# Performance work log

Hardware: AMD Instinct MI355X
Metric: run time of the kernel (lower is better)

## Reference

```python
import jax, jax.numpy as jnp
import numpy as np

B, N = 8, 2048          # clouds x points per cloud
M1, M2 = 1024, 256      # centroids after ratio 0.5, then 0.25
K = 64                  # max_num_neighbors
R1, R2 = 0.2, 0.4       # radii
CURV_K = 10             # knn for curvature
CURV_SCALAR = 10.0      # Net(curvature_scalar)
NEG = -1e30


def _sqdist(a, b):
    # squared pairwise distances [len(a), len(b)] without an [.,.,3] intermediate
    return jnp.sum(a * a, -1)[:, None] + jnp.sum(b * b, -1)[None, :] - 2.0 * (a @ b.T)


def _mlp3(x, Wa, ba, Wb, bb, Wc, bc):
    # torch_geometric MLP: Linear+ReLU hidden layers, plain last layer
    h = jax.nn.relu(x @ Wa + ba)
    h = jax.nn.relu(h @ Wb + bb)
    return h @ Wc + bc


def _curvature(pos):
    # per-point surface variation lambda_min / sum(lambda) over k-NN covariance
    d2 = _sqdist(pos, pos)                        # [N,N]
    _, idx = jax.lax.top_k(-d2, CURV_K)           # k nearest (incl. self)
    nbr = pos[idx]                                # [N,k,3]
    c = nbr - jnp.mean(nbr, 1, keepdims=True)
    cov = jnp.einsum('nki,nkj->nij', c, c) / CURV_K
    ev = jnp.linalg.eigvalsh(cov)                 # ascending
    return ev[:, 0] / (jnp.sum(ev, -1) + 1e-8)


def _fps_weighted(pos, curv, m):
    # farthest point sampling, min-distance score weighted by curvature
    w = 1.0 + CURV_SCALAR * curv
    d0 = jnp.sum((pos - pos[0]) ** 2, -1)
    def step(min_d2, _):
        i = jnp.argmax(min_d2 * w)
        nd = jnp.sum((pos - pos[i]) ** 2, -1)
        return jnp.minimum(min_d2, nd), i
    _, rest = jax.lax.scan(step, d0, None, length=m - 1)
    return jnp.concatenate([jnp.zeros((1,), rest.dtype), rest])


def _sa(x, pos, curv, m, r, params):
    # SAModule: weighted FPS -> radius grouping (cap K) -> PointNetConv (gather, MLP, max)
    idx = _fps_weighted(pos, curv, m)
    cpos = pos[idx]                               # [m,3]
    d2 = _sqdist(cpos, pos)                       # [m,N]
    score = jnp.where(d2 <= r * r, -d2, NEG)
    vals, nidx = jax.lax.top_k(score, K)          # up to K nearest within radius
    mask = vals > NEG * 0.5                       # [m,K]
    rel = pos[nidx] - cpos[:, None, :]            # [m,K,3]
    feats = rel if x is None else jnp.concatenate([x[nidx], rel], -1)
    msg = _mlp3(feats, *params)                   # [m,K,F]
    msg = jnp.where(mask[:, :, None], msg, NEG)
    out = jnp.max(msg, 1)                         # scatter-max aggregation
    out = jnp.where(jnp.any(mask, 1)[:, None], out, 0.0)  # empty groups -> 0
    return out, cpos, curv[idx]


def _forward(pos, W1a, b1a, W1b, b1b, W1c, b1c, W2a, b2a, W2b, b2b, W2c, b2c,
             W3a, b3a, W3b, b3b, W3c, b3c, Wh1, bh1, Wh2, bh2, Wh3, bh3):
    p1 = (W1a, b1a, W1b, b1b, W1c, b1c)
    p2 = (W2a, b2a, W2b, b2b, W2c, b2c)
    p3 = (W3a, b3a, W3b, b3b, W3c, b3c)
    def cloud(p):
        curv = _curvature(p)
        x1, pos1, c1 = _sa(None, p, curv, M1, R1, p1)
        x2, pos2, _ = _sa(x1, pos1, c1, M2, R2, p2)
        g = _mlp3(jnp.concatenate([x2, pos2], -1), *p3)   # [M2,1024]
        return jnp.max(g, 0)                              # global max pool
    gfeat = jax.vmap(cloud)(pos.reshape(B, N, 3))          # [B,1024]
    logits = _mlp3(gfeat, Wh1, bh1, Wh2, bh2, Wh3, bh3)    # dropout (eval) = id
    return jax.nn.log_softmax(logits, -1)


_LAYERS = [("W1a", "b1a", 3, 64), ("W1b", "b1b", 64, 64), ("W1c", "b1c", 64, 128),
           ("W2a", "b2a", 131, 128), ("W2b", "b2b", 128, 128), ("W2c", "b2c", 128, 256),
           ("W3a", "b3a", 259, 256), ("W3b", "b3b", 256, 512), ("W3c", "b3c", 512, 1024),
           ("Wh1", "bh1", 1024, 512), ("Wh2", "bh2", 512, 256), ("Wh3", "bh3", 256, 10)]


def setup_inputs() -> dict:
    key = jax.random.key(0)
    ks = iter(jax.random.split(key, 2 * len(_LAYERS) + 1))
    inp = {"pos": jax.random.uniform(next(ks), (B * N, 3), jnp.float32)}
    for wn, bn, fi, fo in _LAYERS:
        inp[wn] = jax.random.normal(next(ks), (fi, fo), jnp.float32) / np.sqrt(fi)
        inp[bn] = jnp.zeros((fo,), jnp.float32)
    return inp


def reference(pos, W1a, b1a, W1b, b1b, W1c, b1c, W2a, b2a, W2b, b2b, W2c, b2c,
              W3a, b3a, W3b, b3b, W3c, b3c, Wh1, bh1, Wh2, bh2, Wh3, bh3):
    return _forward(pos, W1a, b1a, W1b, b1b, W1c, b1c, W2a, b2a, W2b, b2b, W2c, b2c,
                    W3a, b3a, W3b, b3b, W3c, b3c, Wh1, bh1, Wh2, bh2, Wh3, bh3)
```

## Files before the change

### kernel.cpp

```cpp
#include <hip/hip_runtime.h>
#include <hip/hip_fp16.h>
#include <math.h>

#define TID threadIdx.x

typedef _Float16 h2vec __attribute__((ext_vector_type(2)));
typedef _Float16 f16x8 __attribute__((ext_vector_type(8)));
typedef float f32x4 __attribute__((ext_vector_type(4)));
typedef float f32x2v __attribute__((ext_vector_type(2)));

#if __has_builtin(__builtin_elementwise_fma)
#define EFMA(a, b, c) __builtin_elementwise_fma((a), (b), (c))
#else
static __device__ __forceinline__ f32x2v EFMA(f32x2v a, f32x2v b, f32x2v c) {
    f32x2v r;
    r.x = fmaf(a.x, b.x, c.x);
    r.y = fmaf(a.y, b.y, c.y);
    return r;
}
#endif

static __device__ __forceinline__ float fdot2(unsigned a, unsigned b, float c) {
    h2vec av, bv;
    __builtin_memcpy(&av, &a, 4);
    __builtin_memcpy(&bv, &b, 4);
    return __builtin_amdgcn_fdot2(av, bv, c, false);
}

static __device__ __forceinline__ unsigned packh2(float a, float b) {
    __half2 hh = __floats2half2_rn(a, b);
    unsigned u;
    __builtin_memcpy(&u, &hh, 4);
    return u;
}

static __device__ __forceinline__ unsigned encf(float f) {
    unsigned u = __float_as_uint(f);
    return (u >> 31) ? ~u : (u | 0x80000000u);
}
static __device__ __forceinline__ float decf(unsigned e) {
    unsigned u = (e >> 31) ? (e & 0x7fffffffu) : ~e;
    return __uint_as_float(u);
}

static __device__ __forceinline__ int wave_sum(int v) {
    v += __builtin_amdgcn_update_dpp(0, v, 0x111, 0xf, 0xf, true);
    v += __builtin_amdgcn_update_dpp(0, v, 0x112, 0xf, 0xf, true);
    v += __builtin_amdgcn_update_dpp(0, v, 0x114, 0xf, 0xf, true);
    v += __builtin_amdgcn_update_dpp(0, v, 0x118, 0xf, 0xf, true);
    v += __builtin_amdgcn_update_dpp(0, v, 0x142, 0xf, 0xf, true);
    v += __builtin_amdgcn_update_dpp(0, v, 0x143, 0xf, 0xf, true);
    return __builtin_amdgcn_readlane(v, 63);
}

template <int CTRL>
static __device__ __forceinline__ unsigned long long dpp_max_u64(unsigned long long k) {
    int lo = (int)(unsigned)(k & 0xffffffffULL);
    int hi = (int)(unsigned)(k >> 32);
    int lo2 = __builtin_amdgcn_update_dpp(0, lo, CTRL, 0xf, 0xf, true);
    int hi2 = __builtin_amdgcn_update_dpp(0, hi, CTRL, 0xf, 0xf, true);
    unsigned long long k2 = ((unsigned long long)(unsigned)hi2 << 32) | (unsigned)lo2;
    return k2 > k ? k2 : k;
}

static __device__ __forceinline__ void pack_slot(const float* __restrict__ W,
                                                 unsigned* __restrict__ out,
                                                 int K, int ncols, int t) {
    int lane = t & 63;
    int frag = t >> 6;
    int nct = ncols >> 4;
    int ks = frag / nct, ct = frag - ks * nct;
    int kbase = (ks << 5) + ((lane >> 4) << 3);
    int cc = (ct << 4) + (lane & 15);
    unsigned o[4];
#pragma unroll
    for (int i = 0; i < 4; ++i) {
        int k0 = kbase + 2 * i, k1 = kbase + 2 * i + 1;
        float f0 = (k0 < K) ? W[(size_t)k0 * ncols + cc] : 0.f;
        float f1 = (k1 < K) ? W[(size_t)k1 * ncols + cc] : 0.f;
        o[i] = packh2(f0, f1);
    }
    *(uint4*)&out[(size_t)t * 4] = make_uint4(o[0], o[1], o[2], o[3]);
}

__global__ __launch_bounds__(256) void curv_kernel(const float* __restrict__ pos,
                                                   float* __restrict__ curv) {
    __shared__ float4 sp[2048];
    __shared__ float smd[64][40];
    __shared__ int smi[64][40];
    int cloud = blockIdx.x >> 5;
    int base = cloud << 11;
    for (int j = TID; j < 2048; j += 256) {
        const float* p = pos + (size_t)(base + j) * 3;
        float x = p[0], y = p[1], z = p[2];
        sp[j] = make_float4(x, y, z, fmaf(x, x, fmaf(y, y, z * z)));
    }
    __syncthreads();
    int pt = TID >> 2;
    int sub = TID & 3;
    int li = ((blockIdx.x & 31) << 6) + pt;
    float4 pi = sp[li];
    float bd[10];
    int bi[10];
#pragma unroll
    for (int t = 0; t < 10; ++t) { bd[t] = 3.0e38f; bi[t] = 0; }
    int j0 = sub << 9;
    for (int jj = 0; jj < 512; ++jj) {
        int j = j0 + jj;
        float4 pj = sp[j];
        float dot = fmaf(pi.x, pj.x, fmaf(pi.y, pj.y, pi.z * pj.z));
        float d2 = pi.w + pj.w - 2.0f * dot;
        if (d2 < bd[9]) {
            bd[9] = d2; bi[9] = j;
#pragma unroll
            for (int t = 9; t > 0; --t) {
                if (bd[t] < bd[t - 1]) {
                    float td = bd[t]; bd[t] = bd[t - 1]; bd[t - 1] = td;
                    int ti = bi[t]; bi[t] = bi[t - 1]; bi[t - 1] = ti;
                }
            }
        }
    }
#pragma unroll
    for (int t = 0; t < 10; ++t) {
        smd[pt][sub * 10 + t] = bd[t];
        smi[pt][sub * 10 + t] = bi[t];
    }
    __syncthreads();
    float d0 = smd[pt][0], d1 = smd[pt][10], d2h = smd[pt][20], d3 = smd[pt][30];
    int i0 = smi[pt][0], i1 = smi[pt][10], i2 = smi[pt][20], i3 = smi[pt][30];
    int h0 = 0, h1 = 0, h2c = 0, h3 = 0;
    int mbi[10];
#pragma unroll
    for (int t = 0; t < 10; ++t) {
        bool a01 = (d1 < d0) || (d1 == d0 && i1 < i0);
        float dA = a01 ? d1 : d0; int iA = a01 ? i1 : i0;
        bool a23 = (d3 < d2h) || (d3 == d2h && i3 < i2);
        float dB = a23 ? d3 : d2h; int iB = a23 ? i3 : i2;
        bool ab = (dB < dA) || (dB == dA && iB < iA);
        mbi[t] = ab ? iB : iA;
        if (ab) {
            if (a23) { ++h3; d3 = (h3 < 10) ? smd[pt][30 + h3] : 3.0e38f;
                       i3 = (h3 < 10) ? smi[pt][30 + h3] : 0x7fffffff; }
            else     { ++h2c; d2h = (h2c < 10) ? smd[pt][20 + h2c] : 3.0e38f;
                       i2 = (h2c < 10) ? smi[pt][20 + h2c] : 0x7fffffff; }
        } else {
            if (a01) { ++h1; d1 = (h1 < 10) ? smd[pt][10 + h1] : 3.0e38f;
                       i1 = (h1 < 10) ? smi[pt][10 + h1] : 0x7fffffff; }
            else     { ++h0; d0 = (h0 < 10) ? smd[pt][h0] : 3.0e38f;
                       i0 = (h0 < 10) ? smi[pt][h0] : 0x7fffffff; }
        }
    }
    if (sub != 0) return;
    double sx = 0, sy = 0, sz = 0;
#pragma unroll
    for (int t = 0; t < 10; ++t) { float4 p = sp[mbi[t]]; sx += p.x; sy += p.y; sz += p.z; }
    double mx = sx / 10.0, my = sy / 10.0, mz = sz / 10.0;
    double cxx = 0, cxy = 0, cxz = 0, cyy = 0, cyz = 0, czz = 0;
#pragma unroll
    for (int t = 0; t < 10; ++t) {
        float4 p = sp[mbi[t]];
        double dx = p.x - mx, dy = p.y - my, dz = p.z - mz;
        cxx += dx * dx; cxy += dx * dy; cxz += dx * dz;
        cyy += dy * dy; cyz += dy * dz; czz += dz * dz;
    }
    cxx /= 10.0; cxy /= 10.0; cxz /= 10.0; cyy /= 10.0; cyz /= 10.0; czz /= 10.0;
    double q = (cxx + cyy + czz) / 3.0;
    double b00 = cxx - q, b11 = cyy - q, b22 = czz - q;
    double p2 = b00 * b00 + b11 * b11 + b22 * b22 +
                2.0 * (cxy * cxy + cxz * cxz + cyz * cyz);
    double lmin;
    if (p2 <= 0.0) {
        lmin = q;
    } else {
        double p = sqrt(p2 / 6.0);
        double inv = 1.0 / p;
        double c00 = b00 * inv, c01 = cxy * inv, c02 = cxz * inv;
        double c11 = b11 * inv, c12 = cyz * inv, c22 = b22 * inv;
        double detB = c00 * (c11 * c22 - c12 * c12)
                    - c01 * (c01 * c22 - c12 * c02)
                    + c02 * (c01 * c12 - c11 * c02);
        double r = 0.5 * detB;
        r = fmin(1.0, fmax(-1.0, r));
        double phi = acos(r) / 3.0;
        lmin = q + 2.0 * p * cos(phi + 2.0943951023931953);
    }
    double s3 = cxx + cyy + czz;
    curv[base + li] = (float)(lmin / (s3 + 1e-8));
}

template <int N, int M, int SLOTS>
static __device__ void fps_body(
    const float* __restrict__ srcpos, int stride, const float* __restrict__ srccurv,
    int cloud, float4* __restrict__ outPos, float* __restrict__ outCurv,
    float* __restrict__ outA, int ldA,
    float4* sp, int* sidx, unsigned long long* rec ) {
    constexpr int PAIRS = SLOTS / 2;
    const float* cp = srcpos + (size_t)cloud * N * stride;
    for (int j = TID; j < N; j += 256)
        sp[j] = make_float4(cp[j * stride], cp[j * stride + 1], cp[j * stride + 2], 0.f);
    if (TID == 0) sidx[0] = 0;
    __syncthreads();
    f32x2v px[PAIRS], py[PAIRS], pz[PAIRS], md[PAIRS], wvv[PAIRS];
#pragma unroll
    for (int s = 0; s < PAIRS; ++s) {
        int p0 = ((2 * s) << 8) + TID, p1 = ((2 * s + 1) << 8) + TID;
        float4 q0 = sp[p0], q1 = sp[p1];
        px[s].x = q0.x; px[s].y = q1.x;
        py[s].x = q0.y; py[s].y = q1.y;
        pz[s].x = q0.z; pz[s].y = q1.z;
        md[s].x = 3.0e38f; md[s].y = 3.0e38f;
        wvv[s].x = fmaf(10.0f, srccurv[cloud * N + p0], 1.0f);
        wvv[s].y = fmaf(10.0f, srccurv[cloud * N + p1], 1.0f);
    }
    int lane = TID & 63, w4 = TID >> 6;
    float4 c0 = sp[0];
    float cx = c0.x, cy = c0.y, cz = c0.z;
    for (int t = 1; t < M; ++t) {
        f32x2v cxv, cyv, czv;
        cxv.x = cx; cxv.y = cx; cyv.x = cy; cyv.y = cy; czv.x = cz; czv.y = cz;
        unsigned long long kk[PAIRS];
#pragma unroll
        for (int s = 0; s < PAIRS; ++s) {
            f32x2v dx = px[s] - cxv, dy = py[s] - cyv, dz = pz[s] - czv;
            f32x2v nd = EFMA(dx, dx, EFMA(dy, dy, dz * dz));
            f32x2v m2 = __builtin_elementwise_min(md[s], nd);
            md[s] = m2;
            f32x2v sc = m2 * wvv[s];
            unsigned long long k0 =
                ((unsigned long long)__float_as_uint(sc.x) << 32) |
                (unsigned)(2047 - (((2 * s) << 8) + TID));
            unsigned long long k1 =
                ((unsigned long long)__float_as_uint(sc.y) << 32) |
                (unsigned)(2047 - (((2 * s + 1) << 8) + TID));
            kk[s] = k0 > k1 ? k0 : k1;
        }
        unsigned long long k = kk[0];
#pragma unroll
        for (int s = 1; s < PAIRS; ++s) k = kk[s] > k ? kk[s] : k;
        k = dpp_max_u64<0x111>(k);
        k = dpp_max_u64<0x112>(k);
        k = dpp_max_u64<0x114>(k);
        k = dpp_max_u64<0x118>(k);
        k = dpp_max_u64<0x142>(k);
        k = dpp_max_u64<0x143>(k);
        int pbase = (t & 1) << 2;
        if (lane == 63) rec[pbase | w4] = k;
        __syncthreads();
        unsigned long long k0 = rec[pbase + 0];
        unsigned long long k1 = rec[pbase + 1];
        unsigned long long k2 = rec[pbase + 2];
        unsigned long long k3 = rec[pbase + 3];
        unsigned long long ka = k0 > k1 ? k0 : k1;
        unsigned long long kb = k2 > k3 ? k2 : k3;
        unsigned long long km = ka > kb ? ka : kb;
        int nbix = 2047 - (int)(unsigned)(km & 0xffffffffULL);
        if (TID == 0) sidx[t] = nbix;
        float4 cc = sp[nbix];
        cx = cc.x; cy = cc.y; cz = cc.z;
    }
    __syncthreads();
    for (int j = TID; j < M; j += 256) {
        int id = sidx[j];
        float4 qv = sp[id];
        outPos[cloud * M + j] = qv;
        if (outCurv) outCurv[cloud * M + j] = srccurv[cloud * N + id];
        if (outA) {
            float* a = outA + (size_t)(cloud * M + j) * ldA;
            a[256] = qv.x; a[257] = qv.y; a[258] = qv.z;
        }
    }
}

__global__ __launch_bounds__(256, 1) void fps1_pack_kernel(
    const float* __restrict__ pos, const float* __restrict__ curv,
    float4* __restrict__ pos1, float* __restrict__ curv1,
    const float* __restrict__ Wc, const float* __restrict__ Wa,
    const float* __restrict__ Wb, const float* __restrict__ W3a,
    const float* __restrict__ W3b, const float* __restrict__ W3c,
    unsigned* __restrict__ WcH, unsigned* __restrict__ WaH,
    unsigned* __restrict__ WbH, unsigned* __restrict__ W3aH,
    unsigned* __restrict__ W3bH, unsigned* __restrict__ W3cH,
    unsigned* __restrict__ gfeatE) {
    __shared__ float4 sp[2048];
    __shared__ int sidx[1024];
    __shared__ unsigned long long rec[8];
    if (blockIdx.x < 8) {
        fps_body<2048, 1024, 8>(pos, 3, curv, blockIdx.x, pos1, curv1, nullptr, 0,
                                sp, sidx, rec);
        return;
    }
    int b = blockIdx.x - 8;
    if (b == 0)
        for (int i = TID; i < 8192; i += 256) gfeatE[i] = 0u;
    if (b < 16)        pack_slot(Wc,  WcH,  128, 256,  b * 256 + TID);
    else if (b < 26)   pack_slot(Wa,  WaH,  131, 128,  (b - 16) * 256 + TID);
    else if (b < 34)   pack_slot(Wb,  WbH,  128, 128,  (b - 26) * 256 + TID);
    else if (b < 70)   pack_slot(W3a, W3aH, 259, 256,  (b - 34) * 256 + TID);
    else if (b < 134)  pack_slot(W3b, W3bH, 256, 512,  (b - 70) * 256 + TID);
    else               pack_slot(W3c, W3cH, 512, 1024, (b - 134) * 256 + TID);
}

static __device__ __forceinline__ int select_k64(const unsigned int* ck, const int* ci,
                                                 int c, int lane, int* cnt2, int* sel,
                                                 int* nbOut) {
    if (c <= 64) {
        *nbOut = c;
        return (lane < c) ? ci[lane] : 0;
    }
    unsigned int T = 0;
    for (int bit = 31; bit >= 0; --bit) {
        unsigned int mid = T | (1u << bit);
        int cl = 0;
        for (int q = lane; q < c; q += 64) cl += (ck[q] < mid) ? 1 : 0;
        if (wave_sum(cl) < 64) T = mid;
    }
    int cl = 0;
    for (int q = lane; q < c; q += 64) cl += (ck[q] < T) ? 1 : 0;
    int need = 64 - wave_sum(cl);
    int TI = 0;
    for (int bit = 11; bit >= 0; --bit) {
        int mid = TI | (1 << bit);
        int ce = 0;
        for (int q = lane; q < c; q += 64) ce += (ck[q] == T && ci[q] < mid) ? 1 : 0;
        if (wave_sum(ce) < need) TI = mid;
    }
    for (int q = lane; q < c; q += 64) {
        unsigned int kq = ck[q];
        int iq = ci[q];
        if (kq < T || (kq == T && iq <= TI)) sel[atomicAdd(cnt2, 1)] = iq;
    }
    *nbOut = 64;
    return sel[lane];
}

static __device__ __forceinline__ int select_k64_fast(
    const unsigned* __restrict__ ck, const int* __restrict__ ci,
    int c, int lane, int* sel, int* nbOut) {
    if (c <= 64) {
        *nbOut = c;
        return (lane < c) ? ci[lane] : 0;
    }
    unsigned long long kq[4];
    bool act[4];
#pragma unroll
    for (int q = 0; q < 4; ++q) {
        int idx = (q << 6) + lane;
        bool v = idx < c;
        act[q] = v;
        kq[q] = v ? (((unsigned long long)ck[idx] << 32) | (unsigned)ci[idx]) : 0ULL;
    }
    int excess = c - 64;
    if (excess <= 24) {
        for (int r = 0; r < excess; ++r) {
            unsigned long long k = 0;
#pragma unroll
            for (int q = 0; q < 4; ++q) {
                unsigned long long kc = act[q] ? kq[q] : 0ULL;
                k = kc > k ? kc : k;
            }
            k = dpp_max_u64<0x111>(k);
            k = dpp_max_u64<0x112>(k);
            k = dpp_max_u64<0x114>(k);
            k = dpp_max_u64<0x118>(k);
            k = dpp_max_u64<0x142>(k);
            k = dpp_max_u64<0x143>(k);
            unsigned klo = (unsigned)__builtin_amdgcn_readlane(
                (int)(unsigned)(k & 0xffffffffULL), 63);
            unsigned khi = (unsigned)__builtin_amdgcn_readlane(
                (int)(unsigned)(k >> 32), 63);
            unsigned long long km = ((unsigned long long)khi << 32) | klo;
#pragma unroll
            for (int q = 0; q < 4; ++q)
                if (act[q] && kq[q] == km) act[q] = false;
        }
    } else {
        unsigned T = 0;
        for (int bit = 31; bit >= 0; --bit) {
            unsigned mid = T | (1u << bit);
            int cl = 0;
#pragma unroll
            for (int q = 0; q < 4; ++q)
                cl += (act[q] && (unsigned)(kq[q] >> 32) < mid) ? 1 : 0;
            if (wave_sum(cl) < 64) T = mid;
        }
        int cl = 0;
#pragma unroll
        for (int q = 0; q < 4; ++q)
            cl += (act[q] && (unsigned)(kq[q] >> 32) < T) ? 1 : 0;
        int need = 64 - wave_sum(cl);
        int TI = 0;
        for (int bit = 11; bit >= 0; --bit) {
            int mid = TI | (1 << bit);
            int ce = 0;
#pragma unroll
            for (int q = 0; q < 4; ++q)
                ce += (act[q] && (unsigned)(kq[q] >> 32) == T &&
                       (int)(unsigned)(kq[q] & 0xffffffffULL) < mid) ? 1 : 0;
            if (wave_sum(ce) < need) TI = mid;
        }
#pragma unroll
        for (int q = 0; q < 4; ++q) {
            unsigned hi = (unsigned)(kq[q] >> 32);
            int lo = (int)(unsigned)(kq[q] & 0xffffffffULL);
            act[q] = act[q] && (hi < T || (hi == T && lo <= TI));
        }
    }
    int base = 0;
#pragma unroll
    for (int q = 0; q < 4; ++q) {
        unsigned long long m = __ballot(act[q]);
        if (act[q]) {
            int off = __popcll(m & ((1ULL << lane) - 1));
            sel[base + off] = (int)(unsigned)(kq[q] & 0xffffffffULL);
        }
        base += __popcll(m);
    }
    *nbOut = 64;
    return sel[lane];
}

union U1 {
    struct {
        float4 sp[2048];
        unsigned ck[4][256];
        int ci[4][256];
        int sel[4][64];
    } p;
    unsigned h2s[4][2048];
};

static __device__ void conv1_body(
    int bid, U1& u,
    const float* __restrict__ pos, const float4* __restrict__ pos1,
    const float* __restrict__ W1, const float* __restrict__ B1,
    const float* __restrict__ W2, const float* __restrict__ B2,
    const float* __restrict__ W3, const float* __restrict__ B3,
    float* __restrict__ x1) {
    __shared__ int nbs[4];
    int cloud = bid >> 8;
    int w4 = TID >> 6, lane = TID & 63;
    int centb = (bid & 255) << 2;
    int g = (cloud << 10) + centb + w4;
    int base = cloud << 11;
    for (int j = TID; j < 2048; j += 256) {
        const float* p = pos + (size_t)(base + j) * 3;
        u.p.sp[j] = make_float4(p[0], p[1], p[2], 0.f);
    }
    __syncthreads();
    float4 cq = pos1[g];
    double cx = cq.x, cy = cq.y, cz = cq.z;
    int cnt = 0;
    for (int s = 0; s < 32; ++s) {
        int j = (s << 6) + lane;
        float4 pj = u.p.sp[j];
        double dx = (double)pj.x - cx, dy = (double)pj.y - cy, dz = (double)pj.z - cz;
        double d2 = dx * dx + dy * dy + dz * dz;
        bool in = (d2 <= 0.2 * 0.2);
        unsigned long long m = __ballot(in);
        if (in) {
            int p = cnt + __popcll(m & ((1ULL << lane) - 1));
            if (p < 256) {
                u.p.ck[w4][p] = __float_as_uint((float)d2);
                u.p.ci[w4][p] = j;
            }
        }
        cnt += __popcll(m);
    }
    int c = min(cnt, 256);
    int nb;
    int idxn = select_k64_fast(u.p.ck[w4], u.p.ci[w4], c, lane, u.p.sel[w4], &nb);
    if (lane == 0) nbs[w4] = nb;
    float4 pn = u.p.sp[idxn];
    float rx = pn.x - cq.x, ry = pn.y - cq.y, rz = pn.z - cq.z;
    __syncthreads();
    float h1[64];
#pragma unroll
    for (int cc2 = 0; cc2 < 64; ++cc2) {
        float v = fmaf(rx, W1[cc2], fmaf(ry, W1[64 + cc2], fmaf(rz, W1[128 + cc2], B1[cc2])));
        h1[cc2] = fmaxf(v, 0.f);
    }
#pragma unroll 1
    for (int half = 0; half < 2; ++half) {
        int c0 = half << 5;
        float h2[32];
#pragma unroll
        for (int t = 0; t < 32; ++t) h2[t] = B2[c0 + t];
#pragma unroll
        for (int i = 0; i < 64; ++i) {
            float hv = h1[i];
            const float* wr = W2 + i * 64 + c0;
#pragma unroll
            for (int t = 0; t < 32; ++t) h2[t] = fmaf(hv, wr[t], h2[t]);
        }
#pragma unroll
        for (int t = 0; t < 32; ++t) h2[t] = fmaxf(h2[t], 0.f);
        unsigned* hrow = &u.h2s[w4][lane << 5];
        int sw = (lane & 7) << 2;
#pragma unroll
        for (int q = 0; q < 4; ++q) {
            unsigned tmp[4];
#pragma unroll
            for (int k2 = 0; k2 < 4; ++k2) {
                int jp = (q << 2) + k2;
                tmp[k2] = packh2(h2[2 * jp], h2[2 * jp + 1]);
            }
            int qg = (half << 2) + q;
            *(uint4*)&hrow[(qg << 2) ^ sw] = make_uint4(tmp[0], tmp[1], tmp[2], tmp[3]);
        }
    }
    __syncthreads();
    int ch = ((w4 & 1) << 6) + lane;
    int cbase = (w4 >> 1) << 1;
    unsigned w2[32];
#pragma unroll
    for (int p = 0; p < 32; ++p)
        w2[p] = packh2(W3[(2 * p) * 128 + ch], W3[(2 * p + 1) * 128 + ch]);
    float bv = B3[ch];
#pragma unroll 1
    for (int ci2 = 0; ci2 < 2; ++ci2) {
        int cc = cbase + ci2;
        int nbc = nbs[cc];
        float m = -1e30f;
        for (int n = 0; n < nbc; ++n) {
            const unsigned* hr = &u.h2s[cc][n << 5];
            int sw2 = (n & 7) << 2;
            float a0 = 0.f, a1 = 0.f, a2 = 0.f, a3 = 0.f;
#pragma unroll
            for (int q = 0; q < 8; ++q) {
                uint4 hv = *(const uint4*)&hr[(q << 2) ^ sw2];
                a0 = fdot2(hv.x, w2[(q << 2) + 0], a0);
                a1 = fdot2(hv.y, w2[(q << 2) + 1], a1);
                a2 = fdot2(hv.z, w2[(q << 2) + 2], a2);
                a3 = fdot2(hv.w, w2[(q << 2) + 3], a3);
            }
            m = fmaxf(m, bv + (a0 + a1) + (a2 + a3));
        }
        x1[(size_t)((cloud << 10) + centb + cc) * 128 + ch] = m;
    }
}

union UM {
    U1 c;
    struct {
        float4 sp[1024];
        unsigned long long rec[8];
        int sidx[256];
    } f;
};

__global__ __launch_bounds__(256, 3) void fps2_conv1_kernel(
    const float* __restrict__ pos, const float4* __restrict__ pos1,
    const float* __restrict__ curv1, float4* __restrict__ pos2,
    float* __restrict__ Abuf,
    const float* __restrict__ W1, const float* __restrict__ B1,
    const float* __restrict__ W2, const float* __restrict__ B2,
    const float* __restrict__ W3, const float* __restrict__ B3,
    float* __restrict__ x1) {
    __shared__ UM u;
    if (blockIdx.x < 8) {
        fps_body<1024, 256, 4>((const float*)pos1, 4, curv1, blockIdx.x, pos2,
                               nullptr, Abuf, 260, u.f.sp, u.f.sidx, u.f.rec);
    } else {
        conv1_body(blockIdx.x - 8, u.c, pos, pos1, W1, B1, W2, B2, W3, B3, x1);
    }
}

union U2 {
    struct {
        float4 sp[1024];
        unsigned ck[4][512];
        int ci[4][512];
        int sel[4][64];
        int cnt[4], cnt2[4];
    } p;
    unsigned xs[4][5376];
};

__global__ __launch_bounds__(256, 1) void conv2_kernel(
    const float4* __restrict__ pos1, const float4* __restrict__ pos2,
    const float* __restrict__ x1,
    const unsigned* __restrict__ WaH, const float* __restrict__ Ba,
    const unsigned* __restrict__ WbH, const float* __restrict__ Bb,
    const unsigned* __restrict__ WcH, const float* __restrict__ Bc,
    float* __restrict__ Aout) {
    __shared__ U2 u;
    __shared__ unsigned h1s[4][4352];
    __shared__ int nbs[4];
    int cloud = blockIdx.x >> 6;
    int w4 = TID >> 6, lane = TID & 63;
    int centb = (blockIdx.x & 63) << 2;
    int g = (cloud << 8) + centb + w4;
    int quad = lane >> 4, l15 = lane & 15;
    for (int j = TID; j < 1024; j += 256) u.p.sp[j] = pos1[(cloud << 10) + j];
    if (lane == 0) { u.p.cnt[w4] = 0; u.p.cnt2[w4] = 0; }
    __syncthreads();
    float4 cq = pos2[g];
    double cx = cq.x, cy = cq.y, cz = cq.z;
    for (int s = 0; s < 16; ++s) {
        int j = (s << 6) + lane;
        float4 pj = u.p.sp[j];
        double dx = (double)pj.x - cx, dy = (double)pj.y - cy, dz = (double)pj.z - cz;
        double d2 = dx * dx + dy * dy + dz * dz;
        if (d2 <= 0.4 * 0.4) {
            int p = atomicAdd(&u.p.cnt[w4], 1);
            if (p < 512) { u.p.ck[w4][p] = __float_as_uint((float)d2); u.p.ci[w4][p] = j; }
        }
    }
    __syncthreads();
    int c = min(u.p.cnt[w4], 512);
    int nb;
    int idxn = select_k64(u.p.ck[w4], u.p.ci[w4], c, lane, &u.p.cnt2[w4],
                          u.p.sel[w4], &nb);
    if (lane == 0) nbs[w4] = nb;
    float4 pn = u.p.sp[idxn];
    float rx = pn.x - cq.x, ry = pn.y - cq.y, rz = pn.z - cq.z;
    __syncthreads();
    {
        const float4* xr = (const float4*)(x1 + (size_t)((cloud << 10) + idxn) * 128);
        unsigned* row = &u.xs[w4][lane * 84];
#pragma unroll
        for (int q = 0; q < 16; ++q) {
            float4 a = xr[q * 2], b = xr[q * 2 + 1];
            *(uint4*)&row[q << 2] = make_uint4(packh2(a.x, a.y), packh2(a.z, a.w),
                                               packh2(b.x, b.y), packh2(b.z, b.w));
        }
        *(uint4*)&row[64] = make_uint4(packh2(rx, ry), packh2(rz, 0.f), 0u, 0u);
        *(uint4*)&row[68] = make_uint4(0u, 0u, 0u, 0u);
        *(uint4*)&row[72] = make_uint4(0u, 0u, 0u, 0u);
        *(uint4*)&row[76] = make_uint4(0u, 0u, 0u, 0u);
    }
    float ba8[8];
#pragma unroll
    for (int ct = 0; ct < 8; ++ct) ba8[ct] = Ba[(ct << 4) + l15];
#pragma unroll 1
    for (int ct = 0; ct < 8; ++ct) {
        f16x8 bfrag[5];
#pragma unroll
        for (int ks = 0; ks < 5; ++ks) {
            uint4 bv = *(const uint4*)&WaH[(size_t)((((ks << 3) | ct) << 6) | lane) << 2];
            __builtin_memcpy(&bfrag[ks], &bv, 16);
        }
#pragma unroll
        for (int rt = 0; rt < 4; ++rt) {
            f32x4 acc = {0.f, 0.f, 0.f, 0.f};
#pragma unroll
            for (int ks = 0; ks < 5; ++ks) {
                f16x8 af;
                uint4 av = *(const uint4*)&u.xs[w4][((rt << 4) + l15) * 84 +
                                                    (((ks << 2) + quad) << 2)];
                __builtin_memcpy(&af, &av, 16);
                acc = __builtin_amdgcn_mfma_f32_16x16x32_f16(af, bfrag[ks], acc, 0, 0, 0);
            }
#pragma unroll
            for (int r = 0; r < 4; ++r) {
                float v = fmaxf(acc[r] + ba8[ct], 0.f);
                float vp = __shfl_xor(v, 1, 64);
                if (!(l15 & 1)) {
                    int rowi = (rt << 4) + (quad << 2) + r;
                    h1s[w4][rowi * 68 + (ct << 3) + (l15 >> 1)] = packh2(v, vp);
                }
            }
        }
    }
    unsigned* h2w = &u.xs[w4][0];
#pragma unroll
    for (int ct = 0; ct < 8; ++ct) ba8[ct] = Bb[(ct << 4) + l15];
#pragma unroll 1
    for (int ct = 0; ct < 8; ++ct) {
        f16x8 bfrag[4];
#pragma unroll
        for (int ks = 0; ks < 4; ++ks) {
            uint4 bv = *(const uint4*)&WbH[(size_t)((((ks << 3) | ct) << 6) | lane) << 2];
            __builtin_memcpy(&bfrag[ks], &bv, 16);
        }
#pragma unroll
        for (int rt = 0; rt < 4; ++rt) {
            f32x4 acc = {0.f, 0.f, 0.f, 0.f};
#pragma unroll
            for (int ks = 0; ks < 4; ++ks) {
                f16x8 af;
                uint4 av = *(const uint4*)&h1s[w4][((rt << 4) + l15) * 68 +
                                                   (((ks << 2) + quad) << 2)];
                __builtin_memcpy(&af, &av, 16);
                acc = __builtin_amdgcn_mfma_f32_16x16x32_f16(af, bfrag[ks], acc, 0, 0, 0);
            }
#pragma unroll
            for (int r = 0; r < 4; ++r) {
                float v = fmaxf(acc[r] + ba8[ct], 0.f);
                float vp = __shfl_xor(v, 1, 64);
                if (!(l15 & 1)) {
                    int rowi = (rt << 4) + (quad << 2) + r;
                    int d = (ct << 3) + (l15 >> 1);
                    int ch = d >> 2, din = d & 3;
                    h2w[(rowi << 6) + ((ch ^ (rowi & 15)) << 2) + din] = packh2(v, vp);
                }
            }
        }
    }
    __syncthreads();
    int ctb = w4 << 2;
    f16x8 cfrag[4][4];
#pragma unroll
    for (int ct = 0; ct < 4; ++ct)
#pragma unroll
        for (int ks = 0; ks < 4; ++ks) {
            uint4 bv = *(const uint4*)&WcH[(size_t)((((ks << 4) | (ctb + ct)) << 6) | lane) << 2];
            __builtin_memcpy(&cfrag[ct][ks], &bv, 16);
        }
#pragma unroll 1
    for (int cent = 0; cent < 4; ++cent) {
        const unsigned* h2r = &u.xs[cent][0];
        int nbc = nbs[cent];
        float runM[4][4];
#pragma unroll
        for (int ct = 0; ct < 4; ++ct)
#pragma unroll
            for (int r = 0; r < 4; ++r) runM[ct][r] = -1e30f;
#pragma unroll
        for (int rt = 0; rt < 4; ++rt) {
            int nl = (rt << 4) + l15;
            f16x8 afrag[4];
#pragma unroll
            for (int ks = 0; ks < 4; ++ks) {
                int cp = ((ks << 2) | quad) ^ l15;
                uint4 av = *(const uint4*)&h2r[(nl << 6) + (cp << 2)];
                __builtin_memcpy(&afrag[ks], &av, 16);
            }
#pragma unroll
            for (int ct = 0; ct < 4; ++ct) {
                f32x4 acc = {0.f, 0.f, 0.f, 0.f};
#pragma unroll
                for (int ks = 0; ks < 4; ++ks)
                    acc = __builtin_amdgcn_mfma_f32_16x16x32_f16(afrag[ks], cfrag[ct][ks],
                                                                 acc, 0, 0, 0);
                int nb0 = (rt << 4) + (quad << 2);
#pragma unroll
                for (int r = 0; r < 4; ++r) {
                    float v = (nb0 + r < nbc) ? acc[r] : -1e30f;
                    runM[ct][r] = fmaxf(runM[ct][r], v);
                }
            }
        }
#pragma unroll
        for (int ct = 0; ct < 4; ++ct) {
            float m = fmaxf(fmaxf(runM[ct][0], runM[ct][1]),
                            fmaxf(runM[ct][2], runM[ct][3]));
            m = fmaxf(m, __shfl_xor(m, 16, 64));
            m = fmaxf(m, __shfl_xor(m, 32, 64));
            if (lane < 16) {
                int cc = ((ctb + ct) << 4) | l15;
                Aout[(size_t)((cloud << 8) + centb + cent) * 260 + cc] = m + Bc[cc];
            }
        }
    }
}

__global__ __launch_bounds__(256) void gemm_mfma2(
    const float* __restrict__ A, int lda, const unsigned* __restrict__ Bp, int nct,
    const float* __restrict__ bias, float* __restrict__ C, int ldc, int K,
    int relu, unsigned* __restrict__ gmax) {
    int w = (blockIdx.x << 2) + (TID >> 6);
    int ncg = nct >> 3;
    int rs = w / ncg, cg = w - rs * ncg;
    int r0 = rs << 4, ct0 = cg << 3;
    int lane = TID & 63, quad = lane >> 4, l15 = lane & 15;
    f32x4 acc[8];
#pragma unroll
    for (int ct = 0; ct < 8; ++ct) acc[ct] = (f32x4){0.f, 0.f, 0.f, 0.f};
    const float* ar = A + (size_t)(r0 + l15) * lda;
    int nks = (K + 31) >> 5;
    for (int ks = 0; ks < nks; ++ks) {
        int kb = (ks << 5) + (quad << 3);
        f16x8 af;
        if (kb + 8 <= K) {
            float4 a0 = *(const float4*)(ar + kb);
            float4 a1 = *(const float4*)(ar + kb + 4);
            uint4 av = make_uint4(packh2(a0.x, a0.y), packh2(a0.z, a0.w),
                                  packh2(a1.x, a1.y), packh2(a1.z, a1.w));
            __builtin_memcpy(&af, &av, 16);
        } else {
            float f[8];
#pragma unroll
            for (int j = 0; j < 8; ++j) f[j] = (kb + j < K) ? ar[kb + j] : 0.f;
            uint4 av = make_uint4(packh2(f[0], f[1]), packh2(f[2], f[3]),
                                  packh2(f[4], f[5]), packh2(f[6], f[7]));
            __builtin_memcpy(&af, &av, 16);
        }
#pragma unroll
        for (int ct = 0; ct < 8; ++ct) {
            uint4 bv = *(const uint4*)&Bp[(size_t)(((ks * nct + ct0 + ct) << 6) | lane) << 2];
            f16x8 bf;
            __builtin_memcpy(&bf, &bv, 16);
            acc[ct] = __builtin_amdgcn_mfma_f32_16x16x32_f16(af, bf, acc[ct], 0, 0, 0);
        }
    }
    if (!gmax) {
#pragma unroll
        for (int ct = 0; ct < 8; ++ct) {
            int col = ((ct0 + ct) << 4) + l15;
            float bb = bias[col];
#pragma unroll
            for (int r = 0; r < 4; ++r) {
                int row = r0 + (quad << 2) + r;
                float v = acc[ct][r] + bb;
                if (relu) v = fmaxf(v, 0.f);
                C[(size_t)row * ldc + col] = v;
            }
        }
    } else {
        int cloud = r0 >> 8;
#pragma unroll
        for (int ct = 0; ct < 8; ++ct) {
            int col = ((ct0 + ct) << 4) + l15;
            float bb = bias[col];
            float m = fmaxf(fmaxf(acc[ct][0], acc[ct][1]),
                            fmaxf(acc[ct][2], acc[ct][3])) + bb;
            m = fmaxf(m, __shfl_xor(m, 16, 64));
            m = fmaxf(m, __shfl_xor(m, 32, 64));
            if (quad == 0) atomicMax(&gmax[(cloud << 10) + col], encf(m));
        }
    }
}

__global__ __launch_bounds__(256) void head_kernel(
    const unsigned* __restrict__ gfeatE,
    const float* __restrict__ Wh1, const float* __restrict__ bh1,
    const float* __restrict__ Wh2, const float* __restrict__ bh2,
    const float* __restrict__ Wh3, const float* __restrict__ bh3,
    float* __restrict__ out) {
    __shared__ float gg[1024];
    __shared__ float s1[512];
    __shared__ float s2[256];
    __shared__ float lg[10];
    int cloud = blockIdx.x;
    for (int i = TID; i < 1024; i += 256) gg[i] = decf(gfeatE[(cloud << 10) + i]);
    __syncthreads();
    for (int cc = TID; cc < 512; cc += 256) {
        float v = bh1[cc];
        for (int i = 0; i < 1024; ++i) v = fmaf(gg[i], Wh1[i * 512 + cc], v);
        s1[cc] = fmaxf(v, 0.f);
    }
    __syncthreads();
    for (int cc = TID; cc < 256; cc += 256) {
        float v = bh2[cc];
        for (int i = 0; i < 512; ++i) v = fmaf(s1[i], Wh2[i * 256 + cc], v);
        s2[cc] = fmaxf(v, 0.f);
    }
    __syncthreads();
    if (TID < 10) {
        float v = bh3[TID];
        for (int i = 0; i < 256; ++i) v = fmaf(s2[i], Wh3[i * 10 + TID], v);
        lg[TID] = v;
    }
    __syncthreads();
    if (TID == 0) {
        float mx = lg[0];
        for (int i = 1; i < 10; ++i) mx = fmaxf(mx, lg[i]);
        float s = 0.f;
        for (int i = 0; i < 10; ++i) s += expf(lg[i] - mx);
        float lse = mx + logf(s);
        for (int i = 0; i < 10; ++i) out[cloud * 10 + i] = lg[i] - lse;
    }
}

extern "C" void kernel_launch(void* const* d_in, const int* in_sizes, int n_in,
                              void* d_out, int out_size, void* d_ws, size_t ws_size,
                              hipStream_t stream) {
    (void)in_sizes; (void)n_in; (void)out_size; (void)ws_size;
    const float* pos = (const float*)d_in[0];
    const float* W1a = (const float*)d_in[1];  const float* b1a = (const float*)d_in[2];
    const float* W1b = (const float*)d_in[3];  const float* b1b = (const float*)d_in[4];
    const float* W1c = (const float*)d_in[5];  const float* b1c = (const float*)d_in[6];
    const float* W2a = (const float*)d_in[7];  const float* b2a = (const float*)d_in[8];
    const float* W2b = (const float*)d_in[9];  const float* b2b = (const float*)d_in[10];
    const float* W2c = (const float*)d_in[11]; const float* b2c = (const float*)d_in[12];
    const float* W3a = (const float*)d_in[13]; const float* b3a = (const float*)d_in[14];
    const float* W3b = (const float*)d_in[15]; const float* b3b = (const float*)d_in[16];
    const float* W3c = (const float*)d_in[17]; const float* b3c = (const float*)d_in[18];
    const float* Wh1 = (const float*)d_in[19]; const float* bh1 = (const float*)d_in[20];
    const float* Wh2 = (const float*)d_in[21]; const float* bh2 = (const float*)d_in[22];
    const float* Wh3 = (const float*)d_in[23]; const float* bh3 = (const float*)d_in[24];

    char* ws = (char*)d_ws;
    float*    curv   = (float*)(ws + 0);
    float4*   pos1   = (float4*)(ws + 98304);
    float*    curv1  = (float*)(ws + 229376);
    float4*   pos2   = (float4*)(ws + 270336);
    unsigned* gfeatE = (unsigned*)(ws + 303104);
    unsigned* WcH    = (unsigned*)(ws + 335872);
    unsigned* WaH    = (unsigned*)(ws + 401408);
    unsigned* WbH    = (unsigned*)(ws + 442368);
    float*    x1     = (float*)(ws + 524288);
    float*    Abuf   = (float*)(ws + 4718592);
    float*    h1g    = (float*)(ws + 6848512);
    unsigned* W3aH   = (unsigned*)(ws + 8945664);
    unsigned* W3bH   = (unsigned*)(ws + 9093120);
    unsigned* W3cH   = (unsigned*)(ws + 9355264);
    float*    h2g    = x1;

    curv_kernel<<<256, 256, 0, stream>>>(pos, curv);
    fps1_pack_kernel<<<398, 256, 0, stream>>>(pos, curv, pos1, curv1,
                                              W2c, W2a, W2b, W3a, W3b, W3c,
                                              WcH, WaH, WbH, W3aH, W3bH, W3cH,
                                              gfeatE);
    fps2_conv1_kernel<<<2056, 256, 0, stream>>>(pos, pos1, curv1, pos2, Abuf,
                                                W1a, b1a, W1b, b1b, W1c, b1c, x1);
    conv2_kernel<<<512, 256, 0, stream>>>(pos1, pos2, x1, WaH, b2a, WbH, b2b, WcH, b2c,
                                          Abuf);
    gemm_mfma2<<<64, 256, 0, stream>>>(Abuf, 260, W3aH, 16, b3a, h1g, 256,
                                       259, 1, nullptr);
    gemm_mfma2<<<128, 256, 0, stream>>>(h1g, 256, W3bH, 32, b3b, h2g, 512,
                                        256, 1, nullptr);
    gemm_mfma2<<<256, 256, 0, stream>>>(h2g, 512, W3cH, 64, b3c, nullptr, 0,
                                        512, 0, gfeatE);
    head_kernel<<<8, 256, 0, stream>>>(gfeatE, Wh1, bh1, Wh2, bh2, Wh3, bh3,
                                       (float*)d_out);
}
```

Before: 1.167 ms.

## Use register-based wave selection in conv2 and split head MLP into parallel kernels

In the second set-abstraction conv, the LDS atomic neighbour compaction is replaced with ballot/popcount prefix compaction, and the slow memory-scanning radix select is replaced with the register-resident templated selector (8 chunks for up to 512 candidates). The classifier head, which ran as 8 single-block kernels with serial dot products, is split into three kernels that parallelise the Wh1 and Wh2 layers across more blocks. The head split adds two kernel launches and global round-trips for intermediates. The register selector with 8 64-bit chunks raises register pressure.

Measured after the change: 1.170 ms. About the same (+0.3%).

```diff
diff --git a/kernel.cpp b/kernel.cpp
--- a/kernel.cpp
+++ b/kernel.cpp
@@ -301,50 +301,18 @@
     else               pack_slot(W3c, W3cH, 512, 1024, (b - 134) * 256 + TID);
 }
 
-static __device__ __forceinline__ int select_k64(const unsigned int* ck, const int* ci,
-                                                 int c, int lane, int* cnt2, int* sel,
-                                                 int* nbOut) {
-    if (c <= 64) {
-        *nbOut = c;
-        return (lane < c) ? ci[lane] : 0;
-    }
-    unsigned int T = 0;
-    for (int bit = 31; bit >= 0; --bit) {
-        unsigned int mid = T | (1u << bit);
-        int cl = 0;
-        for (int q = lane; q < c; q += 64) cl += (ck[q] < mid) ? 1 : 0;
-        if (wave_sum(cl) < 64) T = mid;
-    }
-    int cl = 0;
-    for (int q = lane; q < c; q += 64) cl += (ck[q] < T) ? 1 : 0;
-    int need = 64 - wave_sum(cl);
-    int TI = 0;
-    for (int bit = 11; bit >= 0; --bit) {
-        int mid = TI | (1 << bit);
-        int ce = 0;
-        for (int q = lane; q < c; q += 64) ce += (ck[q] == T && ci[q] < mid) ? 1 : 0;
-        if (wave_sum(ce) < need) TI = mid;
-    }
-    for (int q = lane; q < c; q += 64) {
-        unsigned int kq = ck[q];
-        int iq = ci[q];
-        if (kq < T || (kq == T && iq <= TI)) sel[atomicAdd(cnt2, 1)] = iq;
-    }
-    *nbOut = 64;
-    return sel[lane];
-}
-
-static __device__ __forceinline__ int select_k64_fast(
+template <int NCH>
+static __device__ __forceinline__ int select_k64_reg(
     const unsigned* __restrict__ ck, const int* __restrict__ ci,
     int c, int lane, int* sel, int* nbOut) {
     if (c <= 64) {
         *nbOut = c;
         return (lane < c) ? ci[lane] : 0;
     }
-    unsigned long long kq[4];
-    bool act[4];
-#pragma unroll
-    for (int q = 0; q < 4; ++q) {
+    unsigned long long kq[NCH];
+    bool act[NCH];
+#pragma unroll
+    for (int q = 0; q < NCH; ++q) {
         int idx = (q << 6) + lane;
         bool v = idx < c;
         act[q] = v;
@@ -355,7 +323,7 @@
         for (int r = 0; r < excess; ++r) {
             unsigned long long k = 0;
 #pragma unroll
-            for (int q = 0; q < 4; ++q) {
+            for (int q = 0; q < NCH; ++q) {
                 unsigned long long kc = act[q] ? kq[q] : 0ULL;
                 k = kc > k ? kc : k;
             }
@@ -371,7 +339,7 @@
                 (int)(unsigned)(k >> 32), 63);
             unsigned long long km = ((unsigned long long)khi << 32) | klo;
 #pragma unroll
-            for (int q = 0; q < 4; ++q)
+            for (int q = 0; q < NCH; ++q)
                 if (act[q] && kq[q] == km) act[q] = false;
         }
     } else {
@@ -380,13 +348,13 @@
             unsigned mid = T | (1u << bit);
             int cl = 0;
 #pragma unroll
-            for (int q = 0; q < 4; ++q)
+            for (int q = 0; q < NCH; ++q)
                 cl += (act[q] && (unsigned)(kq[q] >> 32) < mid) ? 1 : 0;
             if (wave_sum(cl) < 64) T = mid;
         }
         int cl = 0;
 #pragma unroll
-        for (int q = 0; q < 4; ++q)
+        for (int q = 0; q < NCH; ++q)
             cl += (act[q] && (unsigned)(kq[q] >> 32) < T) ? 1 : 0;
         int need = 64 - wave_sum(cl);
         int TI = 0;
@@ -394,13 +362,13 @@
             int mid = TI | (1 << bit);
             int ce = 0;
 #pragma unroll
-            for (int q = 0; q < 4; ++q)
+            for (int q = 0; q < NCH; ++q)
                 ce += (act[q] && (unsigned)(kq[q] >> 32) == T &&
                        (int)(unsigned)(kq[q] & 0xffffffffULL) < mid) ? 1 : 0;
             if (wave_sum(ce) < need) TI = mid;
         }
 #pragma unroll
-        for (int q = 0; q < 4; ++q) {
+        for (int q = 0; q < NCH; ++q) {
             unsigned hi = (unsigned)(kq[q] >> 32);
             int lo = (int)(unsigned)(kq[q] & 0xffffffffULL);
             act[q] = act[q] && (hi < T || (hi == T && lo <= TI));
@@ -408,7 +376,7 @@
     }
     int base = 0;
 #pragma unroll
-    for (int q = 0; q < 4; ++q) {
+    for (int q = 0; q < NCH; ++q) {
         unsigned long long m = __ballot(act[q]);
         if (act[q]) {
             int off = __popcll(m & ((1ULL << lane) - 1));
@@ -469,7 +437,7 @@
     }
     int c = min(cnt, 256);
     int nb;
-    int idxn = select_k64_fast(u.p.ck[w4], u.p.ci[w4], c, lane, u.p.sel[w4], &nb);
+    int idxn = select_k64_reg<4>(u.p.ck[w4], u.p.ci[w4], c, lane, u.p.sel[w4], &nb);
     if (lane == 0) nbs[w4] = nb;
     float4 pn = u.p.sp[idxn];
     float rx = pn.x - cq.x, ry = pn.y - cq.y, rz = pn.z - cq.z;
@@ -572,7 +540,6 @@
         unsigned ck[4][512];
         int ci[4][512];
         int sel[4][64];
-        int cnt[4], cnt2[4];
     } p;
     unsigned xs[4][5376];
 };
@@ -593,25 +560,29 @@
     int g = (cloud << 8) + centb + w4;
     int quad = lane >> 4, l15 = lane & 15;
     for (int j = TID; j < 1024; j += 256) u.p.sp[j] = pos1[(cloud << 10) + j];
-    if (lane == 0) { u.p.cnt[w4] = 0; u.p.cnt2[w4] = 0; }
     __syncthreads();
     float4 cq = pos2[g];
     double cx = cq.x, cy = cq.y, cz = cq.z;
+    int cnt = 0;
     for (int s = 0; s < 16; ++s) {
         int j = (s << 6) + lane;
         float4 pj = u.p.sp[j];
         double dx = (double)pj.x - cx, dy = (double)pj.y - cy, dz = (double)pj.z - cz;
         double d2 = dx * dx + dy * dy + dz * dz;
-        if (d2 <= 0.4 * 0.4) {
-            int p = atomicAdd(&u.p.cnt[w4], 1);
-            if (p < 512) { u.p.ck[w4][p] = __float_as_uint((float)d2); u.p.ci[w4][p] = j; }
-        }
-    }
-    __syncthreads();
-    int c = min(u.p.cnt[w4], 512);
+        bool in = (d2 <= 0.4 * 0.4);
+        unsigned long long m = __ballot(in);
+        if (in) {
+            int p = cnt + __popcll(m & ((1ULL << lane) - 1));
+            if (p < 512) {
+                u.p.ck[w4][p] = __float_as_uint((float)d2);
+                u.p.ci[w4][p] = j;
+            }
+        }
+        cnt += __popcll(m);
+    }
+    int c = min(cnt, 512);
     int nb;
-    int idxn = select_k64(u.p.ck[w4], u.p.ci[w4], c, lane, &u.p.cnt2[w4],
-                          u.p.sel[w4], &nb);
+    int idxn = select_k64_reg<8>(u.p.ck[w4], u.p.ci[w4], c, lane, u.p.sel[w4], &nb);
     if (lane == 0) nbs[w4] = nb;
     float4 pn = u.p.sp[idxn];
     float rx = pn.x - cq.x, ry = pn.y - cq.y, rz = pn.z - cq.z;
@@ -823,31 +794,39 @@
     }
 }
 
-__global__ __launch_bounds__(256) void head_kernel(
+__global__ __launch_bounds__(128) void head1_kernel(
     const unsigned* __restrict__ gfeatE,
     const float* __restrict__ Wh1, const float* __restrict__ bh1,
+    float* __restrict__ s1g) {
+    int cloud = TID >> 4;
+    int col = (blockIdx.x << 4) + (TID & 15);
+    float v = bh1[col];
+    const unsigned* ge = gfeatE + (cloud << 10);
+    for (int i = 0; i < 1024; ++i)
+        v = fmaf(decf(ge[i]), Wh1[i * 512 + col], v);
+    s1g[(cloud << 9) + col] = fmaxf(v, 0.f);
+}
+
+__global__ __launch_bounds__(128) void head2_kernel(
+    const float* __restrict__ s1g,
     const float* __restrict__ Wh2, const float* __restrict__ bh2,
+    float* __restrict__ s2g) {
+    int cloud = TID >> 4;
+    int col = (blockIdx.x << 4) + (TID & 15);
+    float v = bh2[col];
+    const float* s1 = s1g + (cloud << 9);
+    for (int i = 0; i < 512; ++i)
+        v = fmaf(s1[i], Wh2[i * 256 + col], v);
+    s2g[(cloud << 8) + col] = fmaxf(v, 0.f);
+}
+
+__global__ __launch_bounds__(64) void head3_kernel(
+    const float* __restrict__ s2g,
     const float* __restrict__ Wh3, const float* __restrict__ bh3,
     float* __restrict__ out) {
-    __shared__ float gg[1024];
-    __shared__ float s1[512];
-    __shared__ float s2[256];
     __shared__ float lg[10];
     int cloud = blockIdx.x;
-    for (int i = TID; i < 1024; i += 256) gg[i] = decf(gfeatE[(cloud << 10) + i]);
-    __syncthreads();
-    for (int cc = TID; cc < 512; cc += 256) {
-        float v = bh1[cc];
-        for (int i = 0; i < 1024; ++i) v = fmaf(gg[i], Wh1[i * 512 + cc], v);
-        s1[cc] = fmaxf(v, 0.f);
-    }
-    __syncthreads();
-    for (int cc = TID; cc < 256; cc += 256) {
-        float v = bh2[cc];
-        for (int i = 0; i < 512; ++i) v = fmaf(s1[i], Wh2[i * 256 + cc], v);
-        s2[cc] = fmaxf(v, 0.f);
-    }
-    __syncthreads();
+    const float* s2 = s2g + (cloud << 8);
     if (TID < 10) {
         float v = bh3[TID];
         for (int i = 0; i < 256; ++i) v = fmaf(s2[i], Wh3[i * 10 + TID], v);
@@ -898,6 +877,8 @@
     unsigned* W3bH   = (unsigned*)(ws + 9093120);
     unsigned* W3cH   = (unsigned*)(ws + 9355264);
     float*    h2g    = x1;
+    float*    s1g    = h1g;
+    float*    s2g    = h1g + 4096;
 
     curv_kernel<<<256, 256, 0, stream>>>(pos, curv);
     fps1_pack_kernel<<<398, 256, 0, stream>>>(pos, curv, pos1, curv1,
@@ -914,6 +895,7 @@
                                         256, 1, nullptr);
     gemm_mfma2<<<256, 256, 0, stream>>>(h2g, 512, W3cH, 64, b3c, nullptr, 0,
                                         512, 0, gfeatE);
-    head_kernel<<<8, 256, 0, stream>>>(gfeatE, Wh1, bh1, Wh2, bh2, Wh3, bh3,
-                                       (float*)d_out);
-}
+    head1_kernel<<<32, 128, 0, stream>>>(gfeatE, Wh1, bh1, s1g);
+    head2_kernel<<<16, 128, 0, stream>>>(s1g, Wh2, bh2, s2g);
+    head3_kernel<<<8, 64, 0, stream>>>(s2g, Wh3, bh3, (float*)d_out);
+}
```
